# Performance work log

Measured on AMD Instinct MI355X. Metric: run time of the kernel, lower is better.

The kernel has to match this reference:

```python
import jax, jax.numpy as jnp
import numpy as np

N, F_IN, F_OUT = 32768, 1024, 512
ALPHA = 0.1  # leaky relu slope


def setup_inputs() -> dict:
    key = jax.random.key(0)
    k1, k2, k3, k4, k5 = jax.random.split(key, 5)
    h = jax.random.normal(k1, (1, F_IN), dtype=jnp.float32)
    adj = jax.random.uniform(k2, (N, F_IN), dtype=jnp.float32)
    # xavier-uniform-ish init for W and a, randn for W_1 (matches torch init flavor)
    limW = float(np.sqrt(6.0 / (F_IN + F_OUT)))
    W = jax.random.uniform(k3, (F_IN, F_OUT), minval=-limW, maxval=limW, dtype=jnp.float32)
    lima = float(np.sqrt(6.0 / (2 * F_OUT + 1)))
    a = jax.random.uniform(k4, (2 * F_OUT, 1), minval=-lima, maxval=lima, dtype=jnp.float32)
    W_1 = jax.random.normal(k5, (F_IN, F_OUT), dtype=jnp.float32)
    return {"h": h, "adj": adj, "W": W, "a": a, "W_1": W_1}


def reference(h, adj, W, a, W_1):
    # W_h: [1, Fo]; W_adj: [N, Fo]
    W_h = h @ W
    W_adj = adj @ W
    # Original: cat([W_h.repeat(N,1), W_adj], dim=1) @ a.
    # Equivalent additive decomposition: (W_h @ a1) + (W_adj @ a2) -> no [N, 2Fo] intermediate.
    Fo = W.shape[1]
    a1, a2 = a[:Fo], a[Fo:]
    scores = jax.nn.leaky_relu(W_h @ a1 + W_adj @ a2, negative_slope=ALPHA).squeeze(-1)  # [N]
    attention = jax.nn.softmax(scores)  # softmax over all N rows
    W_adj_transform = adj @ W_1  # [N, Fo]
    out = attention @ W_adj_transform  # [Fo]
    # attention2 in the source: 1 where attention > mean else 0 (as an int mask)
    attention2 = (attention > attention.mean()).astype(jnp.int32)
    return out, attention2
```

## Files before the change

### kernel.cpp

```cpp
#include <hip/hip_runtime.h>

static constexpr int NROWS = 32768;
static constexpr int FIN   = 1024;
static constexpr int FOUT  = 512;
static constexpr int NREP  = 16;


__global__ __launch_bounds__(256) void k1_prep(const float* __restrict__ W,
                                               const float* __restrict__ a,
                                               const float* __restrict__ h,
                                               float* __restrict__ v,
                                               double* __restrict__ hpart) {
    const int k    = (blockIdx.x * blockDim.x + threadIdx.x) >> 6;
    const int lane = threadIdx.x & 63;

    const float4* Wrow = (const float4*)(W + (size_t)k * FOUT);
    float4 w0 = Wrow[lane];
    float4 w1 = Wrow[64 + lane];

    const float4* a4 = (const float4*)a;
    float4 a1_0 = a4[lane];
    float4 a1_1 = a4[64 + lane];
    float4 a2_0 = a4[128 + lane];
    float4 a2_1 = a4[192 + lane];

    double d1 = (double)w0.x * a1_0.x + (double)w0.y * a1_0.y +
                (double)w0.z * a1_0.z + (double)w0.w * a1_0.w +
                (double)w1.x * a1_1.x + (double)w1.y * a1_1.y +
                (double)w1.z * a1_1.z + (double)w1.w * a1_1.w;
    double d2 = (double)w0.x * a2_0.x + (double)w0.y * a2_0.y +
                (double)w0.z * a2_0.z + (double)w0.w * a2_0.w +
                (double)w1.x * a2_1.x + (double)w1.y * a2_1.y +
                (double)w1.z * a2_1.z + (double)w1.w * a2_1.w;

    #pragma unroll
    for (int off = 32; off; off >>= 1) {
        d1 += __shfl_xor(d1, off);
        d2 += __shfl_xor(d2, off);
    }
    if (lane == 0) {
        v[k]     = (float)d2;
        hpart[k] = (double)h[k] * d1;
    }
}

__global__ __launch_bounds__(256) void k2_main(const float* __restrict__ adj,
                                               const float* __restrict__ v,
                                               const double* __restrict__ hpart,
                                               double* __restrict__ e,
                                               float* __restrict__ part,
                                               double* __restrict__ zpart) {
    __shared__ float  uls[4][1024];
    __shared__ double zls[4];

    const int wave  = threadIdx.x >> 6;
    const int lane  = threadIdx.x & 63;
    const int gwave = blockIdx.x * 4 + wave;

    const int row0 = gwave * 8;
    const float4* base = (const float4*)(adj + (size_t)row0 * FIN) + lane;

    float4 A[4], B[4];

    #pragma unroll
    for (int q = 0; q < 4; ++q) A[q] = base[q * 64];
    #pragma unroll
    for (int q = 0; q < 4; ++q) B[q] = base[256 + q * 64];

    double c0 = 0.0;
    #pragma unroll
    for (int j = 0; j < 16; ++j) c0 += hpart[j * 64 + lane];
    #pragma unroll
    for (int off = 32; off; off >>= 1) c0 += __shfl_xor(c0, off);

    const float4* v4 = (const float4*)v;
    float4 vf[4];
    #pragma unroll
    for (int q = 0; q < 4; ++q) vf[q] = v4[q * 64 + lane];

    float  uacc[4][4] = {};
    double zacc = 0.0;

    auto do_row = [&](float4 (&buf)[4], const int r) {
        double dot = 0.0;
        #pragma unroll
        for (int q = 0; q < 4; ++q) {
            dot += (double)buf[q].x * vf[q].x + (double)buf[q].y * vf[q].y +
                   (double)buf[q].z * vf[q].z + (double)buf[q].w * vf[q].w;
        }
        #pragma unroll
        for (int off = 32; off; off >>= 1) dot += __shfl_xor(dot, off);

        double s = c0 + dot;
        if (s < 0.0) s *= 0.1;
        const double ev = exp(s);
        zacc += ev;
        if (lane == 0) e[row0 + r] = ev;

        const float evf = (float)ev;
        #pragma unroll
        for (int q = 0; q < 4; ++q) {
            uacc[q][0] += evf * buf[q].x;
            uacc[q][1] += evf * buf[q].y;
            uacc[q][2] += evf * buf[q].z;
            uacc[q][3] += evf * buf[q].w;
        }

        if (r + 2 < 8) {
            #pragma unroll
            for (int q = 0; q < 4; ++q) buf[q] = base[(r + 2) * 256 + q * 64];
        }
    };

    do_row(A, 0); do_row(B, 1);
    do_row(A, 2); do_row(B, 3);
    do_row(A, 4); do_row(B, 5);
    do_row(A, 6); do_row(B, 7);

    float4* uls4w = (float4*)&uls[wave][0];
    #pragma unroll
    for (int q = 0; q < 4; ++q)
        uls4w[q * 64 + lane] = make_float4(uacc[q][0], uacc[q][1], uacc[q][2], uacc[q][3]);

    if (lane == 0) zls[wave] = zacc;

    __syncthreads();

    const int t = threadIdx.x;
    const float4* uls4 = (const float4*)uls;
    float4 s0 = uls4[t];
    float4 s1 = uls4[256 + t];
    float4 s2 = uls4[512 + t];
    float4 s3 = uls4[768 + t];

    float4* prow = (float4*)(part + (size_t)blockIdx.x * 1024);
    prow[t] = make_float4(s0.x + s1.x + s2.x + s3.x,
                          s0.y + s1.y + s2.y + s3.y,
                          s0.z + s1.z + s2.z + s3.z,
                          s0.w + s1.w + s2.w + s3.w);

    if (t == 0) zpart[blockIdx.x] = zls[0] + zls[1] + zls[2] + zls[3];
}

__global__ __launch_bounds__(256) void k2b_reduce(const float* __restrict__ part,
                                                  float* __restrict__ u16) {
    const int g   = blockIdx.x >> 2;
    const int c   = blockIdx.x & 3;
    const int col = c * 256 + threadIdx.x;
    const float* p = part + (size_t)g * 64 * 1024 + col;
    float acc = 0.f;
    #pragma unroll 8
    for (int b = 0; b < 64; ++b) acc += p[(size_t)b * 1024];
    u16[g * 1024 + col] = acc;
}

__device__ __forceinline__ double block_reduce_Z(const double* __restrict__ zpart,
                                                 double* zs) {
    const int t = threadIdx.x;
    zs[t] = zpart[t] + zpart[256 + t] + zpart[512 + t] + zpart[768 + t];
    __syncthreads();
    for (int st = 128; st > 0; st >>= 1) {
        if (t < st) zs[t] += zs[t + st];
        __syncthreads();
    }
    double Z = zs[0];
    __syncthreads();
    return Z;
}

__global__ __launch_bounds__(256) void k3_final(const double* __restrict__ e,
                                                const double* __restrict__ zpart,
                                                const float* __restrict__ u16,
                                                const float* __restrict__ W1,
                                                float* __restrict__ out) {
    __shared__ double zs[256];
    const double Z = block_reduce_Z(zpart, zs);
    const int t = threadIdx.x;

    if (blockIdx.x < 16) {
        __shared__ float us[1024];
        __shared__ float red[8][32];

        #pragma unroll
        for (int g = 0; g < 4; ++g) {
            const int k = g * 256 + t;
            float s = 0.f;
            #pragma unroll
            for (int rep = 0; rep < NREP; ++rep) s += u16[rep * 1024 + k];
            us[k] = s;
        }
        __syncthreads();

        const int cl  = t & 31;
        const int kg  = t >> 5;
        const int col = blockIdx.x * 32 + cl;
        float acc = 0.f;
        #pragma unroll 8
        for (int kk = 0; kk < 128; ++kk) {
            const int k = kg * 128 + kk;
            acc += us[k] * W1[(size_t)k * FOUT + col];
        }
        red[kg][cl] = acc;
        __syncthreads();
        if (t < 32) {
            float tot = 0.f;
            #pragma unroll
            for (int g = 0; g < 8; ++g) tot += red[g][t];
            out[blockIdx.x * 32 + t] = (float)((double)tot / Z);
        }
    } else {
        const int i0 = (blockIdx.x - 16) * 2048 + t * 8;
        const double2* e2 = (const double2*)(e + i0);
        const double thr = Z;
        float r[8];
        #pragma unroll
        for (int q = 0; q < 4; ++q) {
            double2 ev = e2[q];
            r[2 * q]     = (ev.x * (double)NROWS > thr) ? 1.0f : 0.0f;
            r[2 * q + 1] = (ev.y * (double)NROWS > thr) ? 1.0f : 0.0f;
        }
        float4* o4 = (float4*)(out + FOUT + i0);
        o4[0] = make_float4(r[0], r[1], r[2], r[3]);
        o4[1] = make_float4(r[4], r[5], r[6], r[7]);
    }
}

extern "C" void kernel_launch(void* const* d_in, const int* in_sizes, int n_in,
                              void* d_out, int out_size, void* d_ws, size_t ws_size,
                              hipStream_t stream) {
    const float* h   = (const float*)d_in[0];
    const float* adj = (const float*)d_in[1];
    const float* W   = (const float*)d_in[2];
    const float* a   = (const float*)d_in[3];
    const float* W1  = (const float*)d_in[4];
    float* out = (float*)d_out;

    double* e     = (double*)d_ws;
    double* hpart = e + NROWS;
    double* zpart = hpart + 1024;
    float*  v     = (float*)(zpart + 1024);
    float*  u16   = v + 1024;
    float*  part  = u16 + 16 * 1024;

    k1_prep<<<dim3(256),  dim3(256), 0, stream>>>(W, a, h, v, hpart);
    k2_main<<<dim3(1024), dim3(256), 0, stream>>>(adj, v, hpart, e, part, zpart);
    k2b_reduce<<<dim3(64), dim3(256), 0, stream>>>(part, u16);
    k3_final<<<dim3(32),  dim3(256), 0, stream>>>(e, zpart, u16, W1, out);
}
```

Measured before the change: 217.1 us.

## Load all eight rows up front and reduce row dots through shared memory

Each wave now issues loads for all eight of its adj rows at once into 32 float4 registers instead of double-buffering two rows. Row dot products are no longer reduced with per-row 64-lane shuffle trees: partial sums go to shared memory, are reduced cooperatively across the block, and the first 32 threads compute exp, the row scores, and the block's Z partial. The goal is more memory parallelism and less serialized shuffle work. The cost is heavy register use (128 VGPRs for data plus double accumulators), which may lower occupancy, and extra barriers plus shared memory.

```diff
diff --git a/kernel.cpp b/kernel.cpp
--- a/kernel.cpp
+++ b/kernel.cpp
@@ -51,21 +51,24 @@
                                                float* __restrict__ part,
                                                double* __restrict__ zpart) {
     __shared__ float  uls[4][1024];
-    __shared__ double zls[4];
-
-    const int wave  = threadIdx.x >> 6;
-    const int lane  = threadIdx.x & 63;
-    const int gwave = blockIdx.x * 4 + wave;
-
-    const int row0 = gwave * 8;
+    __shared__ double pd[32][65];
+    __shared__ double red8[32][9];
+    __shared__ float  evs[32];
+
+    const int t    = threadIdx.x;
+    const int wave = t >> 6;
+    const int lane = t & 63;
+    const int rowb = blockIdx.x * 32;
+    const int row0 = rowb + wave * 8;
+
     const float4* base = (const float4*)(adj + (size_t)row0 * FIN) + lane;
 
-    float4 A[4], B[4];
-
-    #pragma unroll
-    for (int q = 0; q < 4; ++q) A[q] = base[q * 64];
-    #pragma unroll
-    for (int q = 0; q < 4; ++q) B[q] = base[256 + q * 64];
+    float4 R[32];
+    #pragma unroll
+    for (int r = 0; r < 8; ++r)
+        #pragma unroll
+        for (int q = 0; q < 4; ++q)
+            R[r * 4 + q] = base[r * 256 + q * 64];
 
     double c0 = 0.0;
     #pragma unroll
@@ -78,55 +81,66 @@
     #pragma unroll
     for (int q = 0; q < 4; ++q) vf[q] = v4[q * 64 + lane];
 
-    float  uacc[4][4] = {};
-    double zacc = 0.0;
-
-    auto do_row = [&](float4 (&buf)[4], const int r) {
+    #pragma unroll
+    for (int r = 0; r < 8; ++r) {
         double dot = 0.0;
         #pragma unroll
         for (int q = 0; q < 4; ++q) {
-            dot += (double)buf[q].x * vf[q].x + (double)buf[q].y * vf[q].y +
-                   (double)buf[q].z * vf[q].z + (double)buf[q].w * vf[q].w;
-        }
-        #pragma unroll
-        for (int off = 32; off; off >>= 1) dot += __shfl_xor(dot, off);
-
+            const float4 dd = R[r * 4 + q];
+            dot += (double)dd.x * vf[q].x + (double)dd.y * vf[q].y +
+                   (double)dd.z * vf[q].z + (double)dd.w * vf[q].w;
+        }
+        pd[wave * 8 + r][lane] = dot;
+    }
+    __syncthreads();
+
+    {
+        const int j = t >> 3;
+        const int o = t & 7;
+        double s8 = 0.0;
+        #pragma unroll
+        for (int i = 0; i < 8; ++i) s8 += pd[j][o * 8 + i];
+        red8[j][o] = s8;
+    }
+    __syncthreads();
+
+    if (t < 32) {
+        double dot = 0.0;
+        #pragma unroll
+        for (int o = 0; o < 8; ++o) dot += red8[t][o];
         double s = c0 + dot;
         if (s < 0.0) s *= 0.1;
         const double ev = exp(s);
-        zacc += ev;
-        if (lane == 0) e[row0 + r] = ev;
-
-        const float evf = (float)ev;
+        e[rowb + t] = ev;
+        evs[t] = (float)ev;
+        double z = ev;
+        #pragma unroll
+        for (int off = 16; off; off >>= 1) z += __shfl_xor(z, off);
+        if (t == 0) zpart[blockIdx.x] = z;
+    }
+    __syncthreads();
+
+    float uacc[4][4] = {};
+    #pragma unroll
+    for (int r = 0; r < 8; ++r) {
+        const float evf = evs[wave * 8 + r];
         #pragma unroll
         for (int q = 0; q < 4; ++q) {
-            uacc[q][0] += evf * buf[q].x;
-            uacc[q][1] += evf * buf[q].y;
-            uacc[q][2] += evf * buf[q].z;
-            uacc[q][3] += evf * buf[q].w;
-        }
-
-        if (r + 2 < 8) {
-            #pragma unroll
-            for (int q = 0; q < 4; ++q) buf[q] = base[(r + 2) * 256 + q * 64];
-        }
-    };
-
-    do_row(A, 0); do_row(B, 1);
-    do_row(A, 2); do_row(B, 3);
-    do_row(A, 4); do_row(B, 5);
-    do_row(A, 6); do_row(B, 7);
+            const float4 dd = R[r * 4 + q];
+            uacc[q][0] += evf * dd.x;
+            uacc[q][1] += evf * dd.y;
+            uacc[q][2] += evf * dd.z;
+            uacc[q][3] += evf * dd.w;
+        }
+    }
 
     float4* uls4w = (float4*)&uls[wave][0];
     #pragma unroll
     for (int q = 0; q < 4; ++q)
         uls4w[q * 64 + lane] = make_float4(uacc[q][0], uacc[q][1], uacc[q][2], uacc[q][3]);
 
-    if (lane == 0) zls[wave] = zacc;
-
-    __syncthreads();
-
-    const int t = threadIdx.x;
+    __syncthreads();
+
     const float4* uls4 = (const float4*)uls;
     float4 s0 = uls4[t];
     float4 s1 = uls4[256 + t];
@@ -138,8 +152,6 @@
                           s0.y + s1.y + s2.y + s3.y,
                           s0.z + s1.z + s2.z + s3.z,
                           s0.w + s1.w + s2.w + s3.w);
-
-    if (t == 0) zpart[blockIdx.x] = zls[0] + zls[1] + zls[2] + zls[3];
 }
 
 __global__ __launch_bounds__(256) void k2b_reduce(const float* __restrict__ part,
```

Result: slower. 221.9 us (+2.2%).
